# Performance work log

Hardware: AMD Instinct MI355X
Metric: run time of the kernel (lower is better)

## Reference

```python
import jax, jax.numpy as jnp
import numpy as np
import math

D_MODEL = 1024
NUM_HEADS = 16
D_K = D_MODEL // NUM_HEADS
MAX_SEQ_LEN = 2048
ROPE_THETA = 10000.0
BATCH = 4
SEQ = 2048


def _rope_buffers():
    inv_freq = 1.0 / (ROPE_THETA ** (jnp.arange(0, D_K, 2, dtype=jnp.float32) / D_K))
    positions = jnp.arange(MAX_SEQ_LEN, dtype=jnp.float32)
    angles = jnp.einsum('i,j->ij', positions, inv_freq)  # [max_seq_len, d_k/2]
    return jnp.cos(angles), jnp.sin(angles)


def setup_inputs() -> dict:
    key = jax.random.key(0)
    kx, kq, kk, kv, ko = jax.random.split(key, 5)
    std = math.sqrt(2.0 / (D_MODEL + D_MODEL))
    x = jax.random.normal(kx, (BATCH, SEQ, D_MODEL), dtype=jnp.float32)
    pos_ids = jnp.broadcast_to(jnp.arange(SEQ, dtype=jnp.int64), (BATCH, SEQ))
    Wq = jax.random.normal(kq, (D_MODEL, D_MODEL), dtype=jnp.float32) * std
    Wk = jax.random.normal(kk, (D_MODEL, D_MODEL), dtype=jnp.float32) * std
    Wv = jax.random.normal(kv, (D_MODEL, D_MODEL), dtype=jnp.float32) * std
    Wo = jax.random.normal(ko, (D_MODEL, D_MODEL), dtype=jnp.float32) * std
    cos, sin = _rope_buffers()
    return {"x": x, "pos_ids": pos_ids, "Wq": Wq, "Wk": Wk, "Wv": Wv, "Wo": Wo, "cos": cos, "sin": sin}


def _apply_rope(t, pos_ids, cos, sin):
    # t: [B, H, S, D_K]; interleaved (even, odd) pair rotation, as in the torch module
    cp = cos[pos_ids][:, None, :, :]  # [B,1,S,D_K/2]
    sp = sin[pos_ids][:, None, :, :]
    tr = t.reshape(*t.shape[:-1], D_K // 2, 2)
    t0, t1 = tr[..., 0], tr[..., 1]
    rot = jnp.stack((t0 * cp - t1 * sp, t0 * sp + t1 * cp), axis=-1)
    return rot.reshape(t.shape)


def reference(x, pos_ids, Wq, Wk, Wv, Wo, cos, sin):
    B, S, _ = x.shape
    def proj(W):
        return jnp.matmul(x, W.T).reshape(B, S, NUM_HEADS, D_K).transpose(0, 2, 1, 3)
    Q = _apply_rope(proj(Wq), pos_ids, cos, sin)
    K = _apply_rope(proj(Wk), pos_ids, cos, sin)
    V = proj(Wv)
    scores = jnp.einsum('bhqd,bhkd->bhqk', Q, K) / math.sqrt(D_K)
    causal = jnp.tril(jnp.ones((S, S), dtype=bool))
    scores = jnp.where(causal, scores, -jnp.inf)
    attn = jax.nn.softmax(scores, axis=-1)
    out = jnp.einsum('bhqk,bhkd->bhqd', attn, V)
    out = out.transpose(0, 2, 1, 3).reshape(B, S, D_MODEL)
    return jnp.matmul(out, Wo.T)
```

## Files before the change

### kernel.cpp

```cpp
#include <hip/hip_runtime.h>
#include <hip/hip_bf16.h>

typedef __bf16 bf16;
typedef __bf16 bf16x4 __attribute__((ext_vector_type(4)));
typedef __bf16 bf16x8 __attribute__((ext_vector_type(8)));
typedef float f32x4 __attribute__((ext_vector_type(4)));
typedef unsigned int u32;

#define BATCH 4
#define SEQN 2048
#define NH 16
#define DK 64
#define DM 1024
#define MROWS (BATCH*SEQN)

__device__ __forceinline__ void async16(bf16* lds, const bf16* g) {
  __builtin_amdgcn_global_load_lds(
      (const __attribute__((address_space(1))) u32*)g,
      (__attribute__((address_space(3))) u32*)lds, 16, 0, 0);
}

__global__ void cvt_all_kernel(const float4* __restrict__ x,  const float4* __restrict__ wq,
                               const float4* __restrict__ wk, const float4* __restrict__ wv,
                               const float4* __restrict__ wo,
                               bf16x4* __restrict__ xb, bf16x4* __restrict__ wqkvb,
                               bf16x4* __restrict__ wob) {
  const int NX = MROWS*DM/4, NW = DM*DM/4;
  int i = blockIdx.x*256 + threadIdx.x;
  const float4* s; bf16x4* d; int j;
  if (i < NX)             { s = x;  d = xb;         j = i; }
  else if (i < NX+NW)     { s = wq; d = wqkvb;      j = i-NX; }
  else if (i < NX+2*NW)   { s = wk; d = wqkvb+NW;   j = i-NX-NW; }
  else if (i < NX+3*NW)   { s = wv; d = wqkvb+2*NW; j = i-NX-2*NW; }
  else if (i < NX+4*NW)   { s = wo; d = wob;        j = i-NX-3*NW; }
  else return;
  float4 f = s[j];
  bf16x4 v;
  v[0] = (bf16)f.x; v[1] = (bf16)f.y; v[2] = (bf16)f.z; v[3] = (bf16)f.w;
  d[j] = v;
}

__device__ __forceinline__ void stage_half(bf16* slot, const bf16* src) {
  const int tid = threadIdx.x; const int w = tid >> 6;
#pragma unroll
  for (int j = 0; j < 2; ++j) {
    int L = j*512 + tid;
    int row = L >> 3;
    int dc  = (L & 7) ^ (row & 7);
    async16(slot + (size_t)(j*512 + w*64)*8, src + (size_t)row*DM + dc*8);
  }
}

#define SBAR() do { __builtin_amdgcn_sched_barrier(0); \
                    __builtin_amdgcn_s_barrier();       \
                    __builtin_amdgcn_sched_barrier(0); } while(0)

#define GPHASE(Ab, Bb, Q, STAGE, FW)  do {                                       \
    bf16x8 afr[2][2];                                                            \
    _Pragma("unroll")                                                            \
    for (int m = 0; m < 2; ++m) {                                                \
      const int row = wm + ((2*(Q)+m)<<4) + lc;                                  \
      _Pragma("unroll")                                                          \
      for (int kk = 0; kk < 2; ++kk)                                             \
        afr[m][kk] = *(const bf16x8*)((Ab) + (size_t)((row<<3) + ((kk*4+quad) ^ (row&7)))*8); \
    }                                                                            \
    if ((Q) == 0) {                                                              \
      _Pragma("unroll")                                                          \
      for (int nt = 0; nt < 4; ++nt) {                                           \
        const int row = wn + (nt<<4) + lc;                                       \
        _Pragma("unroll")                                                        \
        for (int kk = 0; kk < 2; ++kk)                                           \
          bfr[nt][kk] = *(const bf16x8*)((Bb) + (size_t)((row<<3) + ((kk*4+quad) ^ (row&7)))*8); \
      }                                                                          \
    }                                                                            \
    STAGE;                                                                       \
    SBAR();                                                                      \
    asm volatile("s_waitcnt lgkmcnt(0)" ::: "memory");                           \
    __builtin_amdgcn_sched_barrier(0);                                           \
    __builtin_amdgcn_s_setprio(1);                                               \
    _Pragma("unroll")                                                            \
    for (int kk = 0; kk < 2; ++kk)                                               \
      _Pragma("unroll")                                                          \
      for (int m = 0; m < 2; ++m)                                                \
        _Pragma("unroll")                                                        \
        for (int nt = 0; nt < 4; ++nt)                                           \
          acc[2*(Q)+m][nt] = __builtin_amdgcn_mfma_f32_16x16x32_bf16(afr[m][kk], bfr[nt][kk], acc[2*(Q)+m][nt], 0, 0, 0); \
    __builtin_amdgcn_s_setprio(0);                                               \
    FW;                                                                          \
    SBAR();                                                                      \
  } while (0)

__device__ __forceinline__ void gemm_core128x256(const bf16* __restrict__ Ag,
    const bf16* __restrict__ Bg, int r0, int c0, bf16* sm, f32x4 (&acc)[4][4]) {
  const int tid  = threadIdx.x;
  const int lane = tid & 63, quad = lane >> 4, lc = lane & 15;
  const int w = tid >> 6;
  const int wm = (w >> 2)*64, wn = (w & 3)*64;
  const int NT = DM/64;
  bf16* As_[2] = { sm,         sm + 8192  };
  bf16* Bs_[2] = { sm + 16384, sm + 32768 };

  auto stA = [&](int t) {
    stage_half(As_[t&1], Ag + (size_t)r0*DM + t*64);
  };
  auto stB = [&](int t, int h) {
    stage_half(Bs_[t&1] + h*8192, Bg + (size_t)(c0 + h*128)*DM + t*64);
  };

  stB(0,0); stB(0,1); stA(0);
  stB(1,0); stB(1,1);
  asm volatile("s_waitcnt vmcnt(4)" ::: "memory");
  SBAR();

  bf16x8 bfr[4][2];
  for (int X = 0; X < NT/2 - 1; ++X) {
    const int t0 = 2*X;
    GPHASE(As_[0], Bs_[0], 0, stA(t0+1), );
    GPHASE(As_[0], Bs_[0], 1, stB(t0+2,0); stB(t0+2,1), asm volatile("s_waitcnt vmcnt(4)" ::: "memory"));
    GPHASE(As_[1], Bs_[1], 0, stA(t0+2), );
    GPHASE(As_[1], Bs_[1], 1, stB(t0+3,0); stB(t0+3,1), asm volatile("s_waitcnt vmcnt(4)" ::: "memory"));
  }
  GPHASE(As_[0], Bs_[0], 0, stA(NT-1), );
  GPHASE(As_[0], Bs_[0], 1, (void)0, asm volatile("s_waitcnt vmcnt(0)" ::: "memory"));
  GPHASE(As_[1], Bs_[1], 0, (void)0, );
  GPHASE(As_[1], Bs_[1], 1, (void)0, );
}

#define VS 136
__global__ __launch_bounds__(512, 2) void gemm_qkv_kernel(const bf16* __restrict__ A,
    const bf16* __restrict__ Bt, const float* __restrict__ cosb, const float* __restrict__ sinb,
    bf16* __restrict__ Q, bf16* __restrict__ K, bf16* __restrict__ Vt) {
  __shared__ __align__(16) bf16 sm[49152];
  f32x4 acc[4][4] = {};
  const int lin = blockIdx.y * 12 + blockIdx.x;
  const int xcd = lin & 7, j = lin >> 3;
  const int by = xcd*8 + (j & 7), bx = j >> 3;
  const int r0 = by*128, c0 = bx*256;
  gemm_core128x256(A, Bt, r0, c0, sm, acc);
  const int tid  = threadIdx.x;
  const int lane = tid & 63, quad = lane >> 4, lc = lane & 15;
  const int w = tid >> 6;
  const int wm = (w >> 2)*64, wn = (w & 3)*64;
  const int which = c0 >> 10;
  if (which < 2) {
    bf16* T = which == 0 ? Q : K;
#pragma unroll
    for (int mt = 0; mt < 4; ++mt)
#pragma unroll
      for (int r = 0; r < 4; ++r) {
        int gr = r0 + wm + mt*16 + quad*4 + r;
        int b = gr >> 11, s = gr & (SEQN-1);
#pragma unroll
        for (int nt = 0; nt < 4; ++nt) {
          int gc = c0 + wn + nt*16 + lc;
          int c = gc & (DM-1), h = c >> 6, d = c & 63, p = d >> 1;
          float cc = cosb[s*32 + p], ss = sinb[s*32 + p];
          float v  = acc[mt][nt][r];
          float ov = __shfl_xor(v, 1, 64);
          float outv = ((lc & 1) == 0) ? (v*cc - ov*ss) : (ov*ss + v*cc);
          T[(((size_t)(b*NH + h))*SEQN + s)*DK + d] = (bf16)outv;
        }
      }
  } else {
    asm volatile("s_waitcnt vmcnt(0)" ::: "memory");
    __builtin_amdgcn_sched_barrier(0);
    __syncthreads();
#pragma unroll
    for (int mt = 0; mt < 4; ++mt)
#pragma unroll
      for (int nt = 0; nt < 4; ++nt) {
        int col = wn + nt*16 + lc;
        bf16x4 vv;
#pragma unroll
        for (int r = 0; r < 4; ++r) vv[r] = (bf16)acc[mt][nt][r];
        *(bf16x4*)(sm + (size_t)col*VS + wm + mt*16 + quad*4) = vv;
      }
    __syncthreads();
    const int b = r0 >> 11, s_base = r0 & (SEQN-1);
    const int h0 = (c0 & (DM-1)) >> 6;
#pragma unroll
    for (int it = 0; it < 8; ++it) {
      int dall = it*32 + (tid >> 4);
      int s_off = (tid & 15)*8;
      bf16x8 vv = *(const bf16x8*)(sm + (size_t)dall*VS + s_off);
      int h = h0 + (dall >> 6), d = dall & 63;
      *(bf16x8*)(Vt + (((size_t)(b*NH + h))*DK + d)*SEQN + s_base + s_off) = vv;
    }
  }
}

__global__ __launch_bounds__(512, 2) void gemm_out_kernel(const bf16* __restrict__ A,
    const bf16* __restrict__ Bt, float* __restrict__ C) {
  __shared__ __align__(16) bf16 sm[49152];
  f32x4 acc[4][4] = {};
  const int lin = blockIdx.y * 4 + blockIdx.x;
  const int xcd = lin & 7, j = lin >> 3;
  const int by = xcd*8 + (j & 7), bx = j >> 3;
  const int r0 = by*128, c0 = bx*256;
  gemm_core128x256(A, Bt, r0, c0, sm, acc);
  const int tid  = threadIdx.x;
  const int lane = tid & 63, quad = lane >> 4, lc = lane & 15;
  const int w = tid >> 6;
  const int wm = (w >> 2)*64, wn = (w & 3)*64;
#pragma unroll
  for (int mt = 0; mt < 4; ++mt)
#pragma unroll
    for (int nt = 0; nt < 4; ++nt)
#pragma unroll
      for (int r = 0; r < 4; ++r) {
        int gr = r0 + wm + mt*16 + quad*4 + r;
        int gc = c0 + wn + nt*16 + lc;
        C[(size_t)gr*DM + gc] = acc[mt][nt][r];
      }
}

__global__ __launch_bounds__(256, 3) void attn_kernel(const bf16* __restrict__ Q,
    const bf16* __restrict__ K, const bf16* __restrict__ Vt, bf16* __restrict__ Oa) {
  __shared__ __align__(16) bf16 Ks[64*64];
  __shared__ __align__(16) bf16 Vs[64*64];
  __shared__ __align__(16) bf16 Pw[4][32*72];
  const int tid  = threadIdx.x;
  const int w = tid >> 6, lane = tid & 63;
  const int quad = lane >> 4, lc = lane & 15;
  const int bh = blockIdx.x;
  const int yy = blockIdx.y;
  const int sg = yy >> 2, g = yy & 3;
  const int qt = (sg == 0) ? (15 - g) : (sg == 1) ? (8 + g) : (sg == 2) ? (7 - g) : g;
  const int q0 = qt*128;
  const int qr0 = q0 + w*32;
  const bf16* Qp = Q  + (size_t)bh*SEQN*DK;
  const bf16* Kp = K  + (size_t)bh*SEQN*DK;
  const bf16* Vp = Vt + (size_t)bh*DK*SEQN;
  const float SC = 0.125f * 1.44269504f;
  bf16x8 aq[2][2];
#pragma unroll
  for (int mt = 0; mt < 2; ++mt)
#pragma unroll
    for (int kk = 0; kk < 2; ++kk) {
      bf16x8 raw = *(const bf16x8*)(Qp + (size_t)(qr0 + mt*16 + lc)*DK + kk*32 + quad*8);
#pragma unroll
      for (int j = 0; j < 8; ++j) raw[j] = (bf16)((float)raw[j] * SC);
      aq[mt][kk] = raw;
    }
  f32x4 o[2][4] = {};
  float lrow[2][4] = {};
  bf16* P = Pw[w];
  const int nsteps = 2*(qt + 1);

  auto stage = [&](int kt) {
#pragma unroll
    for (int j = 0; j < 2; ++j) {
      int L = j*256 + w*64 + lane;
      int row = L >> 3;
      int s8  = (L & 7) ^ (row & 7);
      bf16* kb = &Ks[(size_t)(j*256 + w*64)*8];
      async16(kb, Kp + (size_t)(kt*64 + row)*DK + s8*8);
      bf16* vb = &Vs[(size_t)(j*256 + w*64)*8];
      async16(vb, Vp + (size_t)row*SEQN + kt*64 + s8*8);
    }
  };

  for (int kt = 0; kt < nsteps; ++kt) {
    const int k0 = kt*64;
    __syncthreads();
    stage(kt);
    asm volatile("s_waitcnt vmcnt(0)" ::: "memory");
    __syncthreads();
    if (k0 <= qr0 + 31) {
      const bf16* Kt = Ks;
      const bf16* Vc = Vs;
      const int lastkey = qr0 + 31;
      f32x4 st[2][4] = {};
#pragma unroll
      for (int kk = 0; kk < 2; ++kk) {
        const int dc = kk*4 + quad;
        bf16x8 bk[4];
#pragma unroll
        for (int nt = 0; nt < 4; ++nt) {
          if (k0 + nt*16 <= lastkey) {
            int kr = nt*16 + lc;
            bk[nt] = *(const bf16x8*)(Kt + (size_t)(kr*8 + (dc ^ (kr & 7)))*8);
          }
        }
#pragma unroll
        for (int nt = 0; nt < 4; ++nt) {
          if (k0 + nt*16 <= lastkey) {
#pragma unroll
            for (int mt = 0; mt < 2; ++mt)
              st[mt][nt] = __builtin_amdgcn_mfma_f32_16x16x32_bf16(aq[mt][kk], bk[nt], st[mt][nt], 0, 0, 0);
          }
        }
      }
#pragma unroll
      for (int mt = 0; mt < 2; ++mt) {
        const int rmin = qr0 + mt*16, rmax = rmin + 15;
#pragma unroll
        for (int nt = 0; nt < 4; ++nt) {
          const int kmin = k0 + nt*16, kmax = kmin + 15;
          f32x4 p;
          if (kmax <= rmin) {
#pragma unroll
            for (int r = 0; r < 4; ++r) p[r] = __builtin_amdgcn_exp2f(st[mt][nt][r]);
          } else if (kmin > rmax) {
            p = f32x4{0.f, 0.f, 0.f, 0.f};
          } else {
            const int key = kmin + lc;
#pragma unroll
            for (int r = 0; r < 4; ++r) {
              float v = __builtin_amdgcn_exp2f(st[mt][nt][r]);
              p[r] = (key > rmin + quad*4 + r) ? 0.f : v;
            }
          }
          st[mt][nt] = p;
#pragma unroll
          for (int r = 0; r < 4; ++r) lrow[mt][r] += p[r];
        }
      }
#pragma unroll
      for (int mt = 0; mt < 2; ++mt)
#pragma unroll
        for (int r = 0; r < 4; ++r)
#pragma unroll
          for (int nt = 0; nt < 4; ++nt)
            P[(mt*16 + quad*4 + r)*72 + nt*16 + lc] = (bf16)st[mt][nt][r];
      asm volatile("s_waitcnt lgkmcnt(0)" ::: "memory");
#pragma unroll
      for (int kk = 0; kk < 2; ++kk) {
        if (k0 + kk*32 <= lastkey) {
          bf16x8 ap[2];
#pragma unroll
          for (int mt = 0; mt < 2; ++mt)
            ap[mt] = *(const bf16x8*)(P + (mt*16 + lc)*72 + kk*32 + quad*8);
          const int kc = kk*4 + quad;
          bf16x8 bv[4];
#pragma unroll
          for (int nb = 0; nb < 4; ++nb) {
            int dr = nb*16 + lc;
            bv[nb] = *(const bf16x8*)(Vc + (size_t)(dr*8 + (kc ^ (dr & 7)))*8);
          }
#pragma unroll
          for (int mt = 0; mt < 2; ++mt)
#pragma unroll
            for (int nb = 0; nb < 4; ++nb)
              o[mt][nb] = __builtin_amdgcn_mfma_f32_16x16x32_bf16(ap[mt], bv[nb], o[mt][nb], 0, 0, 0);
        }
      }
      asm volatile("s_waitcnt lgkmcnt(0)" ::: "memory");
    }
  }
#pragma unroll
  for (int off = 1; off < 16; off <<= 1)
#pragma unroll
    for (int mt = 0; mt < 2; ++mt)
#pragma unroll
      for (int r = 0; r < 4; ++r)
        lrow[mt][r] += __shfl_xor(lrow[mt][r], off, 64);
  const int b = bh >> 4, h = bh & 15;
#pragma unroll
  for (int mt = 0; mt < 2; ++mt)
#pragma unroll
    for (int r = 0; r < 4; ++r) {
      float inv = 1.f / lrow[mt][r];
      int qrow = qr0 + mt*16 + quad*4 + r;
      size_t rowoff = ((size_t)b*SEQN + qrow)*DM + h*DK;
#pragma unroll
      for (int nb = 0; nb < 4; ++nb)
        Oa[rowoff + nb*16 + lc] = (bf16)(o[mt][nb][r]*inv);
    }
}

extern "C" void kernel_launch(void* const* d_in, const int* in_sizes, int n_in,
                              void* d_out, int out_size, void* d_ws, size_t ws_size,
                              hipStream_t stream) {
  const float* x    = (const float*)d_in[0];
  const float* Wq   = (const float*)d_in[2];
  const float* Wk   = (const float*)d_in[3];
  const float* Wv   = (const float*)d_in[4];
  const float* Wo   = (const float*)d_in[5];
  const float* cosb = (const float*)d_in[6];
  const float* sinb = (const float*)d_in[7];
  float* out = (float*)d_out;

  char* ws = (char*)d_ws;
  const size_t SZ_X  = (size_t)MROWS*DM*2;
  const size_t SZ_W  = (size_t)DM*DM*2;
  bf16* xb   = (bf16*)(ws);
  bf16* wqkv = (bf16*)(ws + SZ_X);
  bf16* wo_b = (bf16*)(ws + SZ_X + 3*SZ_W);
  bf16* Qb   = (bf16*)(ws + SZ_X + 4*SZ_W);
  bf16* Kb   = (bf16*)(ws + 2*SZ_X + 4*SZ_W);
  bf16* Vtb  = (bf16*)(ws + 3*SZ_X + 4*SZ_W);
  bf16* Oa   = (bf16*)(ws + 4*SZ_X + 4*SZ_W);

  {
    const int NX = MROWS*DM/4, NW = DM*DM/4;
    int nblk = (NX + 4*NW + 255)/256;
    cvt_all_kernel<<<nblk, 256, 0, stream>>>((const float4*)x, (const float4*)Wq,
        (const float4*)Wk, (const float4*)Wv, (const float4*)Wo,
        (bf16x4*)xb, (bf16x4*)wqkv, (bf16x4*)wo_b);
  }
  gemm_qkv_kernel<<<dim3(3*DM/256, MROWS/128), 512, 0, stream>>>(xb, wqkv, cosb, sinb, Qb, Kb, Vtb);
  attn_kernel<<<dim3(BATCH*NH, SEQN/128), 256, 0, stream>>>(Qb, Kb, Vtb, Oa);
  gemm_out_kernel<<<dim3(DM/256, MROWS/128), 512, 0, stream>>>(Oa, wo_b, out);
}
```

Measured before the change: 245.9 us.

## Transpose QK^T MFMA output for vectorized P stores and simpler row sums

Swaps the MFMA operand order so the score tile comes out transposed: each lane holds four consecutive keys for a single query row. This allows one packed 4-element bf16 store per tile into the P buffer instead of scalar stores, and reduces row-sum tracking to one register per m-tile, with a two-step shuffle plus a broadcast at the end. It also replaces the grouped q-tile ordering with an alternating forward/reverse order based on head parity, which may change load balance across the grid.

Result: slower. 257.5 us (+4.7%).

```diff
diff --git a/kernel.cpp b/kernel.cpp
--- a/kernel.cpp
+++ b/kernel.cpp
@@ -224,8 +224,7 @@
   const int quad = lane >> 4, lc = lane & 15;
   const int bh = blockIdx.x;
   const int yy = blockIdx.y;
-  const int sg = yy >> 2, g = yy & 3;
-  const int qt = (sg == 0) ? (15 - g) : (sg == 1) ? (8 + g) : (sg == 2) ? (7 - g) : g;
+  const int qt = (bh & 1) ? yy : (15 - yy);
   const int q0 = qt*128;
   const int qr0 = q0 + w*32;
   const bf16* Qp = Q  + (size_t)bh*SEQN*DK;
@@ -243,7 +242,7 @@
       aq[mt][kk] = raw;
     }
   f32x4 o[2][4] = {};
-  float lrow[2][4] = {};
+  float lrow[2] = {};
   bf16* P = Pw[w];
   const int nsteps = 2*(qt + 1);
 
@@ -287,13 +286,14 @@
           if (k0 + nt*16 <= lastkey) {
 #pragma unroll
             for (int mt = 0; mt < 2; ++mt)
-              st[mt][nt] = __builtin_amdgcn_mfma_f32_16x16x32_bf16(aq[mt][kk], bk[nt], st[mt][nt], 0, 0, 0);
+              st[mt][nt] = __builtin_amdgcn_mfma_f32_16x16x32_bf16(bk[nt], aq[mt][kk], st[mt][nt], 0, 0, 0);
           }
         }
       }
 #pragma unroll
       for (int mt = 0; mt < 2; ++mt) {
-        const int rmin = qr0 + mt*16, rmax = rmin + 15;
+        const int rmin = qr0 + mt*16;
+        const int qq   = rmin + lc;
 #pragma unroll
         for (int nt = 0; nt < 4; ++nt) {
           const int kmin = k0 + nt*16, kmax = kmin + 15;
@@ -301,28 +301,22 @@
           if (kmax <= rmin) {
 #pragma unroll
             for (int r = 0; r < 4; ++r) p[r] = __builtin_amdgcn_exp2f(st[mt][nt][r]);
-          } else if (kmin > rmax) {
+          } else if (kmin > rmin + 15) {
             p = f32x4{0.f, 0.f, 0.f, 0.f};
           } else {
-            const int key = kmin + lc;
 #pragma unroll
             for (int r = 0; r < 4; ++r) {
               float v = __builtin_amdgcn_exp2f(st[mt][nt][r]);
-              p[r] = (key > rmin + quad*4 + r) ? 0.f : v;
+              p[r] = ((kmin + quad*4 + r) > qq) ? 0.f : v;
             }
           }
-          st[mt][nt] = p;
-#pragma unroll
-          for (int r = 0; r < 4; ++r) lrow[mt][r] += p[r];
-        }
-      }
-#pragma unroll
-      for (int mt = 0; mt < 2; ++mt)
-#pragma unroll
-        for (int r = 0; r < 4; ++r)
-#pragma unroll
-          for (int nt = 0; nt < 4; ++nt)
-            P[(mt*16 + quad*4 + r)*72 + nt*16 + lc] = (bf16)st[mt][nt][r];
+          lrow[mt] += p[0] + p[1] + p[2] + p[3];
+          bf16x4 pw;
+#pragma unroll
+          for (int r = 0; r < 4; ++r) pw[r] = (bf16)p[r];
+          *(bf16x4*)(P + (size_t)(mt*16 + lc)*72 + nt*16 + quad*4) = pw;
+        }
+      }
       asm volatile("s_waitcnt lgkmcnt(0)" ::: "memory");
 #pragma unroll
       for (int kk = 0; kk < 2; ++kk) {
@@ -349,18 +343,17 @@
     }
   }
 #pragma unroll
-  for (int off = 1; off < 16; off <<= 1)
-#pragma unroll
-    for (int mt = 0; mt < 2; ++mt)
-#pragma unroll
-      for (int r = 0; r < 4; ++r)
-        lrow[mt][r] += __shfl_xor(lrow[mt][r], off, 64);
+  for (int mt = 0; mt < 2; ++mt) {
+    lrow[mt] += __shfl_xor(lrow[mt], 16, 64);
+    lrow[mt] += __shfl_xor(lrow[mt], 32, 64);
+  }
   const int b = bh >> 4, h = bh & 15;
 #pragma unroll
   for (int mt = 0; mt < 2; ++mt)
 #pragma unroll
     for (int r = 0; r < 4; ++r) {
-      float inv = 1.f / lrow[mt][r];
+      float rs  = __shfl(lrow[mt], quad*4 + r, 64);
+      float inv = 1.f / rs;
       int qrow = qr0 + mt*16 + quad*4 + r;
       size_t rowoff = ((size_t)b*SEQN + qrow)*DM + h*DK;
 #pragma unroll
```
